# Kernel tuning notes

Hardware: AMD Instinct MI355X
Metric: run time of the kernel (lower is better)

Reference implementation:

```python
import jax, jax.numpy as jnp
import numpy as np


def setup_inputs() -> dict:
    key = jax.random.key(0)
    k1, k2, k3 = jax.random.split(key, 3)
    B, L, D, K = 64, 1024, 768, 1024
    token_embeddings = jax.random.normal(k1, (B, L, D), dtype=jnp.float32)
    gates = jax.random.uniform(k2, (B, L), dtype=jnp.float32)
    attention_mask = jnp.ones((B, L), dtype=jnp.float32)
    centroids = jax.random.normal(k3, (K, D), dtype=jnp.float32)
    return {
        "token_embeddings": token_embeddings,
        "gates": gates,
        "attention_mask": attention_mask,
        "centroids": centroids,
        "entity_cluster": 0,
    }


def reference(token_embeddings, gates, attention_mask, centroids, entity_cluster):
    # ClusterFilter.apply: cdist -> argmin -> entity-cluster gating mask
    B, L, D = token_embeddings.shape
    flat = token_embeddings.reshape(-1, D)                      # [B*L, D]
    # squared Euclidean distances (argmin is invariant to sqrt)
    x2 = jnp.sum(flat * flat, axis=-1, keepdims=True)           # [B*L, 1]
    c2 = jnp.sum(centroids * centroids, axis=-1)                # [K]
    d2 = x2 - 2.0 * (flat @ centroids.T) + c2                   # [B*L, K]
    assignments = jnp.argmin(d2, axis=1).reshape(B, L)          # [B, L]
    entity_mask = (assignments == entity_cluster).astype(gates.dtype)
    entity_mask = entity_mask * attention_mask
    return gates * entity_mask
```

## Files before the change

kernel.cpp:

```cpp
#include <hip/hip_runtime.h>
#include <hip/hip_bf16.h>
#include <stdint.h>

typedef _Float16 half_t;
typedef __attribute__((ext_vector_type(8))) _Float16 half8;
typedef __attribute__((ext_vector_type(4))) _Float16 half4v;
typedef __attribute__((ext_vector_type(4))) float float4v;
typedef unsigned long long u64;

#define D_DIM 768
#define K_CENT 1024
#define M_TOTAL 65536
#define BM 128
#define BN 128
#define BK 64
#define NCHUNK 12
#define NTN 8

#define CLO_OFF   (NTN * NCHUNK * 16384u)
#define C2_OFF    (2u * CLO_OFF)
#define PART_OFF  (C2_OFF + 8192u)

__device__ __forceinline__ uint32_t swz(uint32_t row, uint32_t kbyte) {
  return (row * 128u + kbyte) ^ ((row & 7u) << 4);
}

__device__ __forceinline__ void gll16(const void* g, void* l) {
  __builtin_amdgcn_global_load_lds((const __attribute__((address_space(1))) void*)g,
                                   (__attribute__((address_space(3))) void*)l,
                                   16, 0, 0);
}

__global__ __launch_bounds__(256) void prep_centroids(const float* __restrict__ cent,
                                                      uint8_t* __restrict__ ws) {
  const int n = blockIdx.x;
  const int nt = n >> 7, row = n & 127;
  float ss = 0.f;
  for (int d = threadIdx.x; d < D_DIM; d += 256) {
    float a = cent[n * D_DIM + d];
    ss += a * a;
    half_t hi = (half_t)a;
    half_t lo = (half_t)(a - (float)hi);
    int chunk = d >> 6, k = d & 63;
    uint32_t off = ((uint32_t)(nt * NCHUNK + chunk) << 14) + swz((uint32_t)row, (uint32_t)k * 2u);
    *(half_t*)(ws + off) = hi;
    *(half_t*)(ws + CLO_OFF + off) = lo;
  }
  for (int s = 32; s > 0; s >>= 1) ss += __shfl_down(ss, s, 64);
  __shared__ float red[4];
  if ((threadIdx.x & 63) == 0) red[threadIdx.x >> 6] = ss;
  __syncthreads();
  if (threadIdx.x == 0) {
    float* c2 = (float*)(ws + C2_OFF);
    c2[n] = red[0] + red[1] + red[2] + red[3];
  }
}

__global__ __launch_bounds__(256, 2) void cluster_gemm(const float* __restrict__ X,
                                                       const uint8_t* __restrict__ wsro,
                                                       u64* __restrict__ partial) {
  __shared__ uint8_t smem[65536];
  uint8_t* Ahi = smem;
  uint8_t* Alo = smem + 16384;
  uint8_t* Bhi = smem + 32768;
  uint8_t* Blo = smem + 49152;

  const int bid = blockIdx.x;
  const int L = (bid & 7) * 512 + (bid >> 3);
  const int m_tile = L >> 3;
  const int n_tile = L & 7;
  const int m0 = m_tile * BM;

  const int tid = threadIdx.x;
  const int lane = tid & 63, w = tid >> 6;
  const int wm = w >> 1, wn = w & 1;

  const float* c2p = (const float*)(wsro + C2_OFF);
  const int ncol = n_tile * 128 + wn * 64 + (lane & 15);
  float c2v[4];
#pragma unroll
  for (int n = 0; n < 4; ++n) c2v[n] = c2p[ncol + n * 16];

  float4v acc[4][4];
#pragma unroll
  for (int m = 0; m < 4; ++m)
#pragma unroll
    for (int n = 0; n < 4; ++n) acc[m][n] = (float4v){0.f, 0.f, 0.f, 0.f};

  for (int ch = 0; ch < NCHUNK; ++ch) {
    __syncthreads();
    {
      const uint8_t* srcHi = wsro + (((uint32_t)(n_tile * NCHUNK + ch)) << 14);
      const uint8_t* srcLo = srcHi + CLO_OFF;
      const uint32_t wo = (uint32_t)w << 12;
#pragma unroll
      for (int j = 0; j < 4; ++j) {
        uint32_t off = wo + (uint32_t)j * 1024u;
        gll16(srcHi + off + (lane << 4), Bhi + off);
        gll16(srcLo + off + (lane << 4), Blo + off);
      }
    }
    {
      const int d0 = ch * BK;
#pragma unroll
      for (int i = 0; i < 8; ++i) {
        int f = tid + i * 256;
        int row = f >> 4, c4 = f & 15;
        float4v v = *(const float4v*)(X + (size_t)(m0 + row) * D_DIM + d0 + c4 * 4);
        half4v hi, lo;
#pragma unroll
        for (int jj = 0; jj < 4; ++jj) {
          half_t h = (half_t)v[jj];
          hi[jj] = h;
          lo[jj] = (half_t)(v[jj] - (float)h);
        }
        uint32_t a = swz((uint32_t)row, (uint32_t)c4 * 8u);
        *(half4v*)(Ahi + a) = hi;
        *(half4v*)(Alo + a) = lo;
      }
    }
    __syncthreads();
#pragma unroll
    for (int ks = 0; ks < 2; ++ks) {
      half8 ah[4], al[4], bh[4], bl[4];
      const uint32_t kb = (uint32_t)ks * 64u + (uint32_t)((lane >> 4) << 4);
#pragma unroll
      for (int m = 0; m < 4; ++m) {
        uint32_t row = (uint32_t)(wm * 64 + m * 16 + (lane & 15));
        uint32_t a = swz(row, kb);
        ah[m] = *(const half8*)(Ahi + a);
        al[m] = *(const half8*)(Alo + a);
      }
#pragma unroll
      for (int n = 0; n < 4; ++n) {
        uint32_t row = (uint32_t)(wn * 64 + n * 16 + (lane & 15));
        uint32_t a = swz(row, kb);
        bh[n] = *(const half8*)(Bhi + a);
        bl[n] = *(const half8*)(Blo + a);
      }
#pragma unroll
      for (int m = 0; m < 4; ++m)
#pragma unroll
        for (int n = 0; n < 4; ++n) {
          acc[m][n] = __builtin_amdgcn_mfma_f32_16x16x32_f16(ah[m], bh[n], acc[m][n], 0, 0, 0);
          acc[m][n] = __builtin_amdgcn_mfma_f32_16x16x32_f16(ah[m], bl[n], acc[m][n], 0, 0, 0);
          acc[m][n] = __builtin_amdgcn_mfma_f32_16x16x32_f16(al[m], bh[n], acc[m][n], 0, 0, 0);
        }
    }
  }

  __syncthreads();
  u64* scratch = (u64*)smem;
  const int g = lane >> 4;
#pragma unroll
  for (int m = 0; m < 4; ++m) {
#pragma unroll
    for (int r = 0; r < 4; ++r) {
      u64 key = ~0ull;
#pragma unroll
      for (int n = 0; n < 4; ++n) {
        float s = c2v[n] - 2.0f * acc[m][n][r];
        uint32_t ub = __float_as_uint(s);
        ub ^= (uint32_t)((int32_t)ub >> 31) | 0x80000000u;
        u64 cand = ((u64)ub << 32) | (uint32_t)(ncol + n * 16);
        key = cand < key ? cand : key;
      }
#pragma unroll
      for (int d = 1; d < 16; d <<= 1) {
        u64 o = __shfl_xor(key, d, 64);
        key = o < key ? o : key;
      }
      if ((lane & 15) == 0) {
        int row = wm * 64 + m * 16 + g * 4 + r;
        scratch[row * 2 + wn] = key;
      }
    }
  }
  __syncthreads();
  if (tid < 128) {
    u64 k0 = scratch[tid * 2 + 0], k1 = scratch[tid * 2 + 1];
    partial[(size_t)(m0 + tid) * NTN + n_tile] = k0 < k1 ? k0 : k1;
  }
}

__global__ __launch_bounds__(256) void finalize(const u64* __restrict__ partial,
                                                const float* __restrict__ gates,
                                                const float* __restrict__ att,
                                                const int* __restrict__ ecp,
                                                float* __restrict__ out) {
  int r = blockIdx.x * 256 + threadIdx.x;
  const u64* p = partial + (size_t)r * NTN;
  u64 k = p[0];
#pragma unroll
  for (int j = 1; j < NTN; ++j) { u64 o = p[j]; k = o < k ? o : k; }
  int idx = (int)(uint32_t)k;
  out[r] = gates[r] * att[r] * ((idx == *ecp) ? 1.0f : 0.0f);
}

extern "C" void kernel_launch(void* const* d_in, const int* in_sizes, int n_in,
                              void* d_out, int out_size, void* d_ws, size_t ws_size,
                              hipStream_t stream) {
  const float* X     = (const float*)d_in[0];
  const float* gates = (const float*)d_in[1];
  const float* att   = (const float*)d_in[2];
  const float* cent  = (const float*)d_in[3];
  const int*   ec    = (const int*)d_in[4];
  uint8_t* ws = (uint8_t*)d_ws;
  float* out = (float*)d_out;
  u64* partial = (u64*)(ws + PART_OFF);

  prep_centroids<<<K_CENT, 256, 0, stream>>>(cent, ws);
  cluster_gemm<<<(M_TOTAL / BM) * NTN, 256, 0, stream>>>(X, ws, partial);
  finalize<<<M_TOTAL / 256, 256, 0, stream>>>(partial, gates, att, ec, out);
}
```

Baseline: 537.5 us.

## Double-buffer GEMM tiles with BK=32 and prefetch next chunk during MFMA

Halves the K-chunk to 32 so that two ping-pong LDS buffers fit in the same 64KB. The next chunk's centroid planes are now loaded asynchronously and its X values fetched into registers while the current chunk's MFMAs run. Conversion and stores to LDS happen after compute, with one barrier per iteration. The swizzle is changed to match 64-byte rows and MFMA sections get raised priority. The cost is twice as many barriers and iterations, plus extra registers for the prefetched X values.

```diff
diff --git a/kernel.cpp b/kernel.cpp
--- a/kernel.cpp
+++ b/kernel.cpp
@@ -13,16 +13,18 @@
 #define M_TOTAL 65536
 #define BM 128
 #define BN 128
-#define BK 64
-#define NCHUNK 12
+#define BK 32
+#define NCHUNK 24
 #define NTN 8
 
-#define CLO_OFF   (NTN * NCHUNK * 16384u)
+#define BPLANE 8192u
+
+#define CLO_OFF   (NTN * NCHUNK * BPLANE)
 #define C2_OFF    (2u * CLO_OFF)
 #define PART_OFF  (C2_OFF + 8192u)
 
 __device__ __forceinline__ uint32_t swz(uint32_t row, uint32_t kbyte) {
-  return (row * 128u + kbyte) ^ ((row & 7u) << 4);
+  return (row * 64u + kbyte) ^ (((row >> 1) & 3u) << 4);
 }
 
 __device__ __forceinline__ void gll16(const void* g, void* l) {
@@ -41,8 +43,8 @@
     ss += a * a;
     half_t hi = (half_t)a;
     half_t lo = (half_t)(a - (float)hi);
-    int chunk = d >> 6, k = d & 63;
-    uint32_t off = ((uint32_t)(nt * NCHUNK + chunk) << 14) + swz((uint32_t)row, (uint32_t)k * 2u);
+    int chunk = d >> 5, k = d & 31;
+    uint32_t off = (uint32_t)(nt * NCHUNK + chunk) * BPLANE + swz((uint32_t)row, (uint32_t)k * 2u);
     *(half_t*)(ws + off) = hi;
     *(half_t*)(ws + CLO_OFF + off) = lo;
   }
@@ -60,10 +62,6 @@
                                                        const uint8_t* __restrict__ wsro,
                                                        u64* __restrict__ partial) {
   __shared__ uint8_t smem[65536];
-  uint8_t* Ahi = smem;
-  uint8_t* Alo = smem + 16384;
-  uint8_t* Bhi = smem + 32768;
-  uint8_t* Blo = smem + 49152;
 
   const int bid = blockIdx.x;
   const int L = (bid & 7) * 512 + (bid >> 3);
@@ -87,69 +85,101 @@
 #pragma unroll
     for (int n = 0; n < 4; ++n) acc[m][n] = (float4v){0.f, 0.f, 0.f, 0.f};
 
+  const uint8_t* Bsrc = wsro + (uint32_t)(n_tile * NCHUNK) * BPLANE;
+  const uint32_t wo = (uint32_t)w * 2048u;
+
+  {
+#pragma unroll
+    for (int j = 0; j < 2; ++j) {
+      uint32_t off = wo + (uint32_t)j * 1024u;
+      gll16(Bsrc + off + (lane << 4), smem + 16384u + off);
+      gll16(Bsrc + CLO_OFF + off + (lane << 4), smem + 24576u + off);
+    }
+#pragma unroll
+    for (int i = 0; i < 4; ++i) {
+      int f = tid + i * 256;
+      int row = f >> 3, c4 = f & 7;
+      float4v v = *(const float4v*)(X + (size_t)(m0 + row) * D_DIM + c4 * 4);
+      half4v hi, lo;
+#pragma unroll
+      for (int jj = 0; jj < 4; ++jj) {
+        half_t h = (half_t)v[jj];
+        hi[jj] = h;
+        lo[jj] = (half_t)(v[jj] - (float)h);
+      }
+      uint32_t a = swz((uint32_t)row, (uint32_t)c4 * 8u);
+      *(half4v*)(smem + a) = hi;
+      *(half4v*)(smem + 8192u + a) = lo;
+    }
+    __syncthreads();
+  }
+
+  uint32_t co = 0;
   for (int ch = 0; ch < NCHUNK; ++ch) {
-    __syncthreads();
-    {
-      const uint8_t* srcHi = wsro + (((uint32_t)(n_tile * NCHUNK + ch)) << 14);
-      const uint8_t* srcLo = srcHi + CLO_OFF;
-      const uint32_t wo = (uint32_t)w << 12;
-#pragma unroll
-      for (int j = 0; j < 4; ++j) {
+    const uint32_t nco = co ^ 32768u;
+    float4v apf[4];
+    const bool pf = (ch + 1 < NCHUNK);
+    if (pf) {
+      const uint8_t* sh = Bsrc + (uint32_t)(ch + 1) * BPLANE;
+#pragma unroll
+      for (int j = 0; j < 2; ++j) {
         uint32_t off = wo + (uint32_t)j * 1024u;
-        gll16(srcHi + off + (lane << 4), Bhi + off);
-        gll16(srcLo + off + (lane << 4), Blo + off);
-      }
-    }
-    {
-      const int d0 = ch * BK;
-#pragma unroll
-      for (int i = 0; i < 8; ++i) {
+        gll16(sh + off + (lane << 4), smem + nco + 16384u + off);
+        gll16(sh + CLO_OFF + off + (lane << 4), smem + nco + 24576u + off);
+      }
+      const int d0 = (ch + 1) * BK;
+#pragma unroll
+      for (int i = 0; i < 4; ++i) {
         int f = tid + i * 256;
-        int row = f >> 4, c4 = f & 15;
-        float4v v = *(const float4v*)(X + (size_t)(m0 + row) * D_DIM + d0 + c4 * 4);
+        int row = f >> 3, c4 = f & 7;
+        apf[i] = *(const float4v*)(X + (size_t)(m0 + row) * D_DIM + d0 + c4 * 4);
+      }
+    }
+    half8 ah[4], al[4], bh[4], bl[4];
+    const uint32_t kb = (uint32_t)((lane >> 4) << 4);
+#pragma unroll
+    for (int m = 0; m < 4; ++m) {
+      uint32_t a = co + swz((uint32_t)(wm * 64 + m * 16 + (lane & 15)), kb);
+      ah[m] = *(const half8*)(smem + a);
+      al[m] = *(const half8*)(smem + 8192u + a);
+    }
+#pragma unroll
+    for (int n = 0; n < 4; ++n) {
+      uint32_t a = co + swz((uint32_t)(wn * 64 + n * 16 + (lane & 15)), kb);
+      bh[n] = *(const half8*)(smem + 16384u + a);
+      bl[n] = *(const half8*)(smem + 24576u + a);
+    }
+    __builtin_amdgcn_s_setprio(1);
+#pragma unroll
+    for (int m = 0; m < 4; ++m)
+#pragma unroll
+      for (int n = 0; n < 4; ++n) {
+        acc[m][n] = __builtin_amdgcn_mfma_f32_16x16x32_f16(ah[m], bh[n], acc[m][n], 0, 0, 0);
+        acc[m][n] = __builtin_amdgcn_mfma_f32_16x16x32_f16(ah[m], bl[n], acc[m][n], 0, 0, 0);
+        acc[m][n] = __builtin_amdgcn_mfma_f32_16x16x32_f16(al[m], bh[n], acc[m][n], 0, 0, 0);
+      }
+    __builtin_amdgcn_s_setprio(0);
+    if (pf) {
+#pragma unroll
+      for (int i = 0; i < 4; ++i) {
+        int f = tid + i * 256;
+        int row = f >> 3, c4 = f & 7;
         half4v hi, lo;
 #pragma unroll
         for (int jj = 0; jj < 4; ++jj) {
-          half_t h = (half_t)v[jj];
+          half_t h = (half_t)apf[i][jj];
           hi[jj] = h;
-          lo[jj] = (half_t)(v[jj] - (float)h);
+          lo[jj] = (half_t)(apf[i][jj] - (float)h);
         }
         uint32_t a = swz((uint32_t)row, (uint32_t)c4 * 8u);
-        *(half4v*)(Ahi + a) = hi;
-        *(half4v*)(Alo + a) = lo;
+        *(half4v*)(smem + nco + a) = hi;
+        *(half4v*)(smem + nco + 8192u + a) = lo;
       }
     }
     __syncthreads();
-#pragma unroll
-    for (int ks = 0; ks < 2; ++ks) {
-      half8 ah[4], al[4], bh[4], bl[4];
-      const uint32_t kb = (uint32_t)ks * 64u + (uint32_t)((lane >> 4) << 4);
-#pragma unroll
-      for (int m = 0; m < 4; ++m) {
-        uint32_t row = (uint32_t)(wm * 64 + m * 16 + (lane & 15));
-        uint32_t a = swz(row, kb);
-        ah[m] = *(const half8*)(Ahi + a);
-        al[m] = *(const half8*)(Alo + a);
-      }
-#pragma unroll
-      for (int n = 0; n < 4; ++n) {
-        uint32_t row = (uint32_t)(wn * 64 + n * 16 + (lane & 15));
-        uint32_t a = swz(row, kb);
-        bh[n] = *(const half8*)(Bhi + a);
-        bl[n] = *(const half8*)(Blo + a);
-      }
-#pragma unroll
-      for (int m = 0; m < 4; ++m)
-#pragma unroll
-        for (int n = 0; n < 4; ++n) {
-          acc[m][n] = __builtin_amdgcn_mfma_f32_16x16x32_f16(ah[m], bh[n], acc[m][n], 0, 0, 0);
-          acc[m][n] = __builtin_amdgcn_mfma_f32_16x16x32_f16(ah[m], bl[n], acc[m][n], 0, 0, 0);
-          acc[m][n] = __builtin_amdgcn_mfma_f32_16x16x32_f16(al[m], bh[n], acc[m][n], 0, 0, 0);
-        }
-    }
-  }
-
-  __syncthreads();
+    co = nco;
+  }
+
   u64* scratch = (u64*)smem;
   const int g = lane >> 4;
 #pragma unroll
```

New measurement: 534.6 us. No clear change (-0.5%).

## Use 256x256 double-buffered tiles with interleaved load/MFMA ping-pong schedule

Applied to the files above, without the earlier changes.

Enlarges the GEMM block tile to 256x256 with BK=32 and 512 threads (8 waves, each owning 128x64 outputs). LDS is double-buffered in 128KB of dynamic shared memory, and the B prefetch, A global loads and fp16 hi/lo split writes for the next k-step are interleaved with four MFMA quadrants separated by barriers. s_setprio is raised around the MFMA bursts. The aim is to hide global and LDS latency behind matrix math and raise arithmetic intensity per loaded byte. The cost is fewer blocks per CU because of the large LDS footprint, more barriers, and higher register pressure from 32 accumulator tiles.

```diff
diff --git a/kernel.cpp b/kernel.cpp
--- a/kernel.cpp
+++ b/kernel.cpp
@@ -11,18 +11,21 @@
 #define D_DIM 768
 #define K_CENT 1024
 #define M_TOTAL 65536
-#define BM 128
-#define BN 128
-#define BK 64
-#define NCHUNK 12
-#define NTN 8
-
-#define CLO_OFF   (NTN * NCHUNK * 16384u)
-#define C2_OFF    (2u * CLO_OFF)
-#define PART_OFF  (C2_OFF + 8192u)
+#define BM 256
+#define BN 256
+#define BK 32
+#define NT 24
+#define NTN 4
+
+#define BPLANE 16384u
+
+#define CLO_OFF  (NTN * NT * BPLANE)
+#define C2_OFF   (2u * CLO_OFF)
+#define PART_OFF (C2_OFF + 8192u)
+
 
 __device__ __forceinline__ uint32_t swz(uint32_t row, uint32_t kbyte) {
-  return (row * 128u + kbyte) ^ ((row & 7u) << 4);
+  return (row * 64u + kbyte) ^ (((row >> 1) & 3u) << 4);
 }
 
 __device__ __forceinline__ void gll16(const void* g, void* l) {
@@ -34,15 +37,15 @@
 __global__ __launch_bounds__(256) void prep_centroids(const float* __restrict__ cent,
                                                       uint8_t* __restrict__ ws) {
   const int n = blockIdx.x;
-  const int nt = n >> 7, row = n & 127;
+  const int nt = n >> 8, row = n & 255;
   float ss = 0.f;
   for (int d = threadIdx.x; d < D_DIM; d += 256) {
     float a = cent[n * D_DIM + d];
     ss += a * a;
     half_t hi = (half_t)a;
     half_t lo = (half_t)(a - (float)hi);
-    int chunk = d >> 6, k = d & 63;
-    uint32_t off = ((uint32_t)(nt * NCHUNK + chunk) << 14) + swz((uint32_t)row, (uint32_t)k * 2u);
+    int chunk = d >> 5, k = d & 31;
+    uint32_t off = (uint32_t)(nt * NT + chunk) * BPLANE + swz((uint32_t)row, (uint32_t)k * 2u);
     *(half_t*)(ws + off) = hi;
     *(half_t*)(ws + CLO_OFF + off) = lo;
   }
@@ -56,104 +59,115 @@
   }
 }
 
-__global__ __launch_bounds__(256, 2) void cluster_gemm(const float* __restrict__ X,
+__global__ __launch_bounds__(512, 2) void cluster_gemm(const float* __restrict__ X,
                                                        const uint8_t* __restrict__ wsro,
                                                        u64* __restrict__ partial) {
-  __shared__ uint8_t smem[65536];
-  uint8_t* Ahi = smem;
-  uint8_t* Alo = smem + 16384;
-  uint8_t* Bhi = smem + 32768;
-  uint8_t* Blo = smem + 49152;
+  extern __shared__ uint8_t smem[];
 
   const int bid = blockIdx.x;
-  const int L = (bid & 7) * 512 + (bid >> 3);
-  const int m_tile = L >> 3;
-  const int n_tile = L & 7;
+  const int L = (bid & 7) * 128 + (bid >> 3);
+  const int m_tile = L >> 2, n_tile = L & 3;
   const int m0 = m_tile * BM;
 
   const int tid = threadIdx.x;
   const int lane = tid & 63, w = tid >> 6;
-  const int wm = w >> 1, wn = w & 1;
+  const int wm = w >> 2, wn = w & 3;
+  const uint32_t kb = (uint32_t)((lane >> 4) << 4);
 
   const float* c2p = (const float*)(wsro + C2_OFF);
-  const int ncol = n_tile * 128 + wn * 64 + (lane & 15);
+  const int ncol = n_tile * 256 + wn * 64 + (lane & 15);
   float c2v[4];
 #pragma unroll
   for (int n = 0; n < 4; ++n) c2v[n] = c2p[ncol + n * 16];
 
-  float4v acc[4][4];
-#pragma unroll
-  for (int m = 0; m < 4; ++m)
+  float4v acc[8][4];
+#pragma unroll
+  for (int m = 0; m < 8; ++m)
 #pragma unroll
     for (int n = 0; n < 4; ++n) acc[m][n] = (float4v){0.f, 0.f, 0.f, 0.f};
 
-  for (int ch = 0; ch < NCHUNK; ++ch) {
-    __syncthreads();
-    {
-      const uint8_t* srcHi = wsro + (((uint32_t)(n_tile * NCHUNK + ch)) << 14);
-      const uint8_t* srcLo = srcHi + CLO_OFF;
-      const uint32_t wo = (uint32_t)w << 12;
-#pragma unroll
-      for (int j = 0; j < 4; ++j) {
-        uint32_t off = wo + (uint32_t)j * 1024u;
-        gll16(srcHi + off + (lane << 4), Bhi + off);
-        gll16(srcLo + off + (lane << 4), Blo + off);
-      }
-    }
-    {
-      const int d0 = ch * BK;
-#pragma unroll
-      for (int i = 0; i < 8; ++i) {
-        int f = tid + i * 256;
-        int row = f >> 4, c4 = f & 15;
-        float4v v = *(const float4v*)(X + (size_t)(m0 + row) * D_DIM + d0 + c4 * 4);
-        half4v hi, lo;
-#pragma unroll
-        for (int jj = 0; jj < 4; ++jj) {
-          half_t h = (half_t)v[jj];
-          hi[jj] = h;
-          lo[jj] = (half_t)(v[jj] - (float)h);
-        }
-        uint32_t a = swz((uint32_t)row, (uint32_t)c4 * 8u);
-        *(half4v*)(Ahi + a) = hi;
-        *(half4v*)(Alo + a) = lo;
-      }
-    }
-    __syncthreads();
-#pragma unroll
-    for (int ks = 0; ks < 2; ++ks) {
-      half8 ah[4], al[4], bh[4], bl[4];
-      const uint32_t kb = (uint32_t)ks * 64u + (uint32_t)((lane >> 4) << 4);
-#pragma unroll
-      for (int m = 0; m < 4; ++m) {
-        uint32_t row = (uint32_t)(wm * 64 + m * 16 + (lane & 15));
-        uint32_t a = swz(row, kb);
-        ah[m] = *(const half8*)(Ahi + a);
-        al[m] = *(const half8*)(Alo + a);
-      }
-#pragma unroll
-      for (int n = 0; n < 4; ++n) {
-        uint32_t row = (uint32_t)(wn * 64 + n * 16 + (lane & 15));
-        uint32_t a = swz(row, kb);
-        bh[n] = *(const half8*)(Bhi + a);
-        bl[n] = *(const half8*)(Blo + a);
-      }
-#pragma unroll
-      for (int m = 0; m < 4; ++m)
-#pragma unroll
-        for (int n = 0; n < 4; ++n) {
-          acc[m][n] = __builtin_amdgcn_mfma_f32_16x16x32_f16(ah[m], bh[n], acc[m][n], 0, 0, 0);
-          acc[m][n] = __builtin_amdgcn_mfma_f32_16x16x32_f16(ah[m], bl[n], acc[m][n], 0, 0, 0);
-          acc[m][n] = __builtin_amdgcn_mfma_f32_16x16x32_f16(al[m], bh[n], acc[m][n], 0, 0, 0);
-        }
-    }
-  }
-
-  __syncthreads();
+  float4v apf[4];
+  half8 ah[4], al[4], bh0[2], bl0[2], bh1[2], bl1[2];
+
+#define A_LOAD(T1) { const int d0 = (T1) * BK;                                        \
+  _Pragma("unroll") for (int i = 0; i < 4; ++i) {                                     \
+    int f = tid + i * 512; int row = f >> 3, c4 = f & 7;                              \
+    apf[i] = *(const float4v*)(X + (size_t)(m0 + row) * D_DIM + d0 + c4 * 4); } }
+
+#define A_WRITE(DB) { _Pragma("unroll") for (int i = 0; i < 4; ++i) {                 \
+    int f = tid + i * 512; int row = f >> 3, c4 = f & 7;                              \
+    half4v hi, lo;                                                                    \
+    _Pragma("unroll") for (int j = 0; j < 4; ++j) {                                   \
+      half_t h = (half_t)apf[i][j]; hi[j] = h; lo[j] = (half_t)(apf[i][j] - (float)h);} \
+    uint32_t a = (DB) + swz((uint32_t)row, (uint32_t)c4 * 8u);                        \
+    *(half4v*)(smem + a) = hi; *(half4v*)(smem + a + 16384u) = lo; } }
+
+#define B_GLL_HI(T1, DB) { const uint8_t* s_ = wsro + (uint32_t)(n_tile * NT + (T1)) * BPLANE; \
+    uint32_t o_ = (uint32_t)w * 2048u;                                                \
+    gll16(s_ + o_ + (lane << 4), smem + (DB) + o_);                                   \
+    gll16(s_ + o_ + 1024u + (lane << 4), smem + (DB) + o_ + 1024u); }
+
+#define B_GLL_LO(T1, DB) { const uint8_t* s_ = wsro + CLO_OFF + (uint32_t)(n_tile * NT + (T1)) * BPLANE; \
+    uint32_t o_ = (uint32_t)w * 2048u;                                                \
+    gll16(s_ + o_ + (lane << 4), smem + (DB) + 16384u + o_);                          \
+    gll16(s_ + o_ + 1024u + (lane << 4), smem + (DB) + 16384u + o_ + 1024u); }
+
+#define READ_A(HALF, AB) { _Pragma("unroll") for (int m = 0; m < 4; ++m) {            \
+    uint32_t a = (AB) + swz((uint32_t)(wm * 128 + ((HALF) * 4 + m) * 16 + (lane & 15)), kb); \
+    ah[m] = *(const half8*)(smem + a); al[m] = *(const half8*)(smem + a + 16384u); } }
+
+#define READ_B(NH, BB, BH, BL) { _Pragma("unroll") for (int n = 0; n < 2; ++n) {      \
+    uint32_t a = (BB) + swz((uint32_t)(wn * 64 + ((NH) * 2 + n) * 16 + (lane & 15)), kb); \
+    BH[n] = *(const half8*)(smem + a); BL[n] = *(const half8*)(smem + a + 16384u); } }
+
+#define MFMA_Q(MB, NB, BH, BL) { __builtin_amdgcn_s_setprio(1);                       \
+  _Pragma("unroll") for (int m = 0; m < 4; ++m)                                       \
+  _Pragma("unroll") for (int n = 0; n < 2; ++n) {                                     \
+    float4v* A_ = &acc[(MB) + m][(NB) + n];                                           \
+    *A_ = __builtin_amdgcn_mfma_f32_16x16x32_f16(ah[m], BH[n], *A_, 0, 0, 0);         \
+    *A_ = __builtin_amdgcn_mfma_f32_16x16x32_f16(ah[m], BL[n], *A_, 0, 0, 0);         \
+    *A_ = __builtin_amdgcn_mfma_f32_16x16x32_f16(al[m], BH[n], *A_, 0, 0, 0); }       \
+  __builtin_amdgcn_s_setprio(0); }
+
+#define BAR() __builtin_amdgcn_s_barrier()
+
+  uint32_t Ab = 0u, Bb = 65536u;
+
+  A_LOAD(0);
+  B_GLL_HI(0, Bb); B_GLL_LO(0, Bb);
+  A_WRITE(Ab);
+  asm volatile("s_waitcnt vmcnt(0) lgkmcnt(0)" ::: "memory");
+  BAR();
+
+  for (int t = 0; t < NT; ++t) {
+    const uint32_t AbN = Ab ^ 32768u, BbN = Bb ^ 32768u;
+    const bool st = (t + 1 < NT);
+    if (st) { A_LOAD(t + 1); B_GLL_HI(t + 1, BbN); }
+    READ_A(0, Ab);
+    READ_B(0, Bb, bh0, bl0);
+    BAR();
+    MFMA_Q(0, 0, bh0, bl0);
+    BAR();
+    if (st) { B_GLL_LO(t + 1, BbN); }
+    READ_B(1, Bb, bh1, bl1);
+    BAR();
+    MFMA_Q(0, 2, bh1, bl1);
+    BAR();
+    READ_A(1, Ab);
+    BAR();
+    MFMA_Q(4, 2, bh1, bl1);
+    BAR();
+    if (st) { A_WRITE(AbN); }
+    MFMA_Q(4, 0, bh0, bl0);
+    asm volatile("s_waitcnt vmcnt(0) lgkmcnt(0)" ::: "memory");
+    BAR();
+    Ab = AbN; Bb = BbN;
+  }
+
   u64* scratch = (u64*)smem;
   const int g = lane >> 4;
 #pragma unroll
-  for (int m = 0; m < 4; ++m) {
+  for (int m = 0; m < 8; ++m) {
 #pragma unroll
     for (int r = 0; r < 4; ++r) {
       u64 key = ~0ull;
@@ -171,15 +185,17 @@
         key = o < key ? o : key;
       }
       if ((lane & 15) == 0) {
-        int row = wm * 64 + m * 16 + g * 4 + r;
-        scratch[row * 2 + wn] = key;
+        int row = wm * 128 + m * 16 + g * 4 + r;
+        scratch[row * 4 + wn] = key;
       }
     }
   }
   __syncthreads();
-  if (tid < 128) {
-    u64 k0 = scratch[tid * 2 + 0], k1 = scratch[tid * 2 + 1];
-    partial[(size_t)(m0 + tid) * NTN + n_tile] = k0 < k1 ? k0 : k1;
+  if (tid < 256) {
+    u64 k = scratch[tid * 4];
+#pragma unroll
+    for (int j = 1; j < 4; ++j) { u64 o = scratch[tid * 4 + j]; k = o < k ? o : k; }
+    partial[(size_t)(m0 + tid) * NTN + n_tile] = k;
   }
 }
 
@@ -209,7 +225,10 @@
   float* out = (float*)d_out;
   u64* partial = (u64*)(ws + PART_OFF);
 
+  hipFuncSetAttribute((const void*)cluster_gemm,
+                      hipFuncAttributeMaxDynamicSharedMemorySize, 131072);
+
   prep_centroids<<<K_CENT, 256, 0, stream>>>(cent, ws);
-  cluster_gemm<<<(M_TOTAL / BM) * NTN, 256, 0, stream>>>(X, ws, partial);
+  cluster_gemm<<<(M_TOTAL / BM) * NTN, 512, 131072, stream>>>(X, ws, partial);
   finalize<<<M_TOTAL / 256, 256, 0, stream>>>(partial, gates, att, ec, out);
 }
```

Measured after the change: 490.5 us. -8.7%, faster.
